# Kernel optimization log

Measured on AMD Instinct MI355X. Metric: run time of the kernel, lower is better.

## Reference

```python
import jax, jax.numpy as jnp
import numpy as np

B, C, H, W = 2, 512, 64, 64
TC = 256  # transform_channels


def _w(k, o, i):
    return jax.random.normal(k, (o, i), jnp.float32) * (1.0 / np.sqrt(i))


def setup_inputs() -> dict:
    key = jax.random.key(0)
    ks = jax.random.split(key, 8)
    ones = lambda n: jnp.ones((n,), jnp.float32)
    zeros = lambda n: jnp.zeros((n,), jnp.float32)
    return {
        "x": jax.random.normal(ks[0], (B, C, H, W), jnp.float32),
        "q_w1": _w(ks[1], TC, C), "q_g1": ones(TC), "q_b1": zeros(TC),
        "q_w2": _w(ks[2], TC, TC), "q_g2": ones(TC), "q_b2": zeros(TC),
        "k_w1": _w(ks[3], TC, 2 * C), "k_g1": ones(TC), "k_b1": zeros(TC),
        "k_w2": _w(ks[4], TC, TC), "k_g2": ones(TC), "k_b2": zeros(TC),
        "v_w": _w(ks[5], TC, 2 * C), "v_g": ones(TC), "v_b": zeros(TC),
        "o_w": _w(ks[6], C, TC), "o_g": ones(C), "o_b": zeros(C),
    }


def _proj(x, w, g, b):
    """1x1 conv (bias-free) + eval-mode BN (mean=0,var=1 -> per-ch affine) + ReLU.
    x: (B, Cin, N) -> (B, Cout, N)"""
    y = jnp.einsum('oc,bcn->bon', w, x)
    return jax.nn.relu(y * g[None, :, None] + b[None, :, None])


def reference(x, q_w1, q_g1, q_b1, q_w2, q_g2, q_b2,
              k_w1, k_g1, k_b1, k_w2, k_g2, k_b2,
              v_w, v_g, v_b, o_w, o_g, o_b):
    b, c, h, w = x.shape
    n = h * w
    xf = x.reshape(b, c, n)
    # image-level context: spatial softmax * feats, averaged over all positions
    g_vec = jnp.mean(jax.nn.softmax(xf, axis=2) * xf, axis=2)        # (b, c)
    g_map = jnp.broadcast_to(g_vec[:, :, None], (b, c, n))           # 1x1 bilinear upsample == broadcast
    kv_in = jnp.concatenate([g_map, xf], axis=1)                     # (b, 2c, n)

    q = _proj(_proj(xf, q_w1, q_g1, q_b1), q_w2, q_g2, q_b2)         # (b, tc, n)
    k = _proj(_proj(kv_in, k_w1, k_g1, k_b1), k_w2, k_g2, k_b2)      # (b, tc, n)
    v = _proj(kv_in, v_w, v_g, v_b)                                  # (b, tc, n)

    tc = q.shape[1]
    sim = jnp.einsum('bcn,bcm->bnm', q, k) * (tc ** -0.5)            # (b, n, n)
    attn = jax.nn.softmax(sim, axis=-1)
    ctx = jnp.einsum('bnm,bcm->bcn', attn, v)                        # (b, tc, n)
    out = _proj(ctx, o_w, o_g, o_b)                                  # (b, c, n)
    return out.reshape(b, -1, h, w)
```

## Files before the change

### kernel.cpp

```cpp
#include <hip/hip_runtime.h>
#include <stdint.h>

#define DEVINL __device__ __forceinline__

typedef short s16x8 __attribute__((ext_vector_type(8)));
typedef short s16x4 __attribute__((ext_vector_type(4)));
typedef float f32x4 __attribute__((ext_vector_type(4)));
typedef int   i32x4 __attribute__((ext_vector_type(4)));

DEVINL f32x4 MFMA16(s16x8 a, s16x8 b, f32x4 c) {
  return __builtin_amdgcn_mfma_f32_16x16x32_bf16(a, b, c, 0, 0, 0);
}

DEVINL short f2bf(float f) {
  uint32_t u = __float_as_uint(f);
  uint32_t r = (u + 0x7fffu + ((u >> 16) & 1u)) >> 16;
  return (short)r;
}

DEVINL int packbf(float a, float b) {
  return (int)((uint32_t)(uint16_t)f2bf(a) | ((uint32_t)(uint16_t)f2bf(b) << 16));
}

DEVINL int ab_off(int row, int kg) {
  return ((row * 128 + kg * 16) ^ ((row & 7) << 4)) >> 1;
}
DEVINL int k_off(int key, int dg) {
  return ((key * 512 + dg * 16) ^ ((key & 7) << 4)) >> 1;
}

__global__ __launch_bounds__(256) void prep_kernel(
    const float* __restrict__ x,
    const float* __restrict__ qw1, const float* __restrict__ qw2,
    const float* __restrict__ kw1, const float* __restrict__ kw2,
    const float* __restrict__ vw, const float* __restrict__ ow,
    short* __restrict__ wbuf, short* __restrict__ xt, float* __restrict__ g) {
  __shared__ float t[32][33];
  int gblk = blockIdx.x, tid = threadIdx.x;
  if (gblk < 2560) {
    int idx = gblk * 256 + tid;
    const float* src; int base, stride, coloff, sh, mask;
    if (idx < 131072)      { src = qw1; base = 0;      stride = 512;  coloff = 0;   sh = 9; mask = 511; }
    else if (idx < 196608) { src = qw2; base = 131072; stride = 256;  coloff = 0;   sh = 8; mask = 255; }
    else if (idx < 327680) { src = kw1; base = 196608; stride = 1024; coloff = 512; sh = 9; mask = 511; }
    else if (idx < 393216) { src = kw2; base = 327680; stride = 256;  coloff = 0;   sh = 8; mask = 255; }
    else if (idx < 524288) { src = vw;  base = 393216; stride = 1024; coloff = 512; sh = 9; mask = 511; }
    else                   { src = ow;  base = 524288; stride = 256;  coloff = 0;   sh = 8; mask = 255; }
    int l = idx - base;
    int r = l >> sh, c = l & mask;
    wbuf[idx] = f2bf(src[(size_t)r * stride + coloff + c]);
  } else if (gblk < 6656) {
    int g2 = gblk - 2560;
    int nt = g2 & 127, ct = (g2 >> 7) & 15, b = g2 >> 11;
    int tx = tid & 31, ty = tid >> 5;
    for (int i = 0; i < 4; ++i) {
      int c = ct * 32 + ty + i * 8;
      t[ty + i * 8][tx] = x[((size_t)(b * 512 + c)) * 4096 + nt * 32 + tx];
    }
    __syncthreads();
    for (int i = 0; i < 4; ++i) {
      int n = nt * 32 + ty + i * 8;
      xt[((size_t)(b * 4096 + n)) * 512 + ct * 32 + tx] = f2bf(t[tx][ty + i * 8]);
    }
  } else {
    int g3 = gblk - 6656;
    int c = g3 & 511, b = g3 >> 9;
    const float* row = x + ((size_t)(b * 512 + c)) * 4096;
    int w = tid >> 6, lane = tid & 63;
    float vals[16];
    float vmax = -3e38f;
    for (int i = 0; i < 4; ++i) {
      float4 v = ((const float4*)row)[tid + i * 256];
      vals[i * 4 + 0] = v.x; vals[i * 4 + 1] = v.y;
      vals[i * 4 + 2] = v.z; vals[i * 4 + 3] = v.w;
    }
    for (int i = 0; i < 16; ++i) vmax = fmaxf(vmax, vals[i]);
    for (int off = 1; off < 64; off <<= 1) vmax = fmaxf(vmax, __shfl_xor(vmax, off));
    float* sb = &t[0][0];
    if (lane == 0) sb[w] = vmax;
    __syncthreads();
    vmax = fmaxf(fmaxf(sb[0], sb[1]), fmaxf(sb[2], sb[3]));
    float se = 0.f, sex = 0.f;
    for (int i = 0; i < 16; ++i) {
      float e = __expf(vals[i] - vmax);
      se += e; sex += e * vals[i];
    }
    for (int off = 1; off < 64; off <<= 1) {
      se += __shfl_xor(se, off);
      sex += __shfl_xor(sex, off);
    }
    __syncthreads();
    if (lane == 0) { sb[4 + w] = se; sb[8 + w] = sex; }
    __syncthreads();
    if (tid == 0) {
      float tse = sb[4] + sb[5] + sb[6] + sb[7];
      float tsx = sb[8] + sb[9] + sb[10] + sb[11];
      g[b * 512 + c] = tsx / (tse * 4096.0f);
    }
  }
}

__global__ __launch_bounds__(64) void bias_kernel(const float* __restrict__ kw1,
                                                  const float* __restrict__ vw,
                                                  const float* __restrict__ g,
                                                  float* __restrict__ kbias,
                                                  float* __restrict__ vbias) {
  int o = blockIdx.x, b = blockIdx.y, which = blockIdx.z;
  const float* W = which ? vw : kw1;
  int lane = threadIdx.x;
  float s = 0.f;
  for (int j = 0; j < 8; ++j) {
    int c = lane + j * 64;
    s += W[(size_t)o * 1024 + c] * g[b * 512 + c];
  }
  for (int off = 1; off < 64; off <<= 1) s += __shfl_xor(s, off);
  if (lane == 0) (which ? vbias : kbias)[b * 256 + o] = s;
}

DEVINL void gemm_core(const short* __restrict__ Ap, const short* __restrict__ Bp,
                      int K, short* Alds, short* Blds, int tid,
                      f32x4 (&acc)[4][2]) {
  int lane = tid & 63, w = tid >> 6, lg = lane >> 4, ln = lane & 15;
  int wm = w & 1, wn = w >> 1;
  int nk = K >> 6;
  for (int kt = 0; kt < nk; ++kt) {
    int k0 = kt * 64;
#pragma unroll
    for (int j = 0; j < 4; ++j) {
      int c = tid + j * 256;
      int row = c >> 3, kg = c & 7;
      *(s16x8*)(Alds + ab_off(row, kg)) =
          *(const s16x8*)(Ap + (size_t)row * K + k0 + kg * 8);
    }
#pragma unroll
    for (int j = 0; j < 2; ++j) {
      int c = tid + j * 256;
      int row = c >> 3, kg = c & 7;
      *(s16x8*)(Blds + ab_off(row, kg)) =
          *(const s16x8*)(Bp + (size_t)row * K + k0 + kg * 8);
    }
    __syncthreads();
#pragma unroll
    for (int ks = 0; ks < 2; ++ks) {
      s16x8 af[4], bfr[2];
#pragma unroll
      for (int mi = 0; mi < 4; ++mi)
        af[mi] = *(const s16x8*)(Alds + ab_off(wm * 64 + mi * 16 + ln, ks * 4 + lg));
#pragma unroll
      for (int nj = 0; nj < 2; ++nj)
        bfr[nj] = *(const s16x8*)(Blds + ab_off(wn * 32 + nj * 16 + ln, ks * 4 + lg));
#pragma unroll
      for (int mi = 0; mi < 4; ++mi)
#pragma unroll
        for (int nj = 0; nj < 2; ++nj)
          acc[mi][nj] = MFMA16(af[mi], bfr[nj], acc[mi][nj]);
    }
    __syncthreads();
  }
}

__global__ __launch_bounds__(256) void gemm_l1(
    const short* __restrict__ xt,
    const short* __restrict__ WQ1, const short* __restrict__ WK1,
    const short* __restrict__ WV,
    const float* __restrict__ qg1, const float* __restrict__ qb1,
    const float* __restrict__ kg1, const float* __restrict__ kb1,
    const float* __restrict__ vg, const float* __restrict__ vb,
    const float* __restrict__ kbias, const float* __restrict__ vbias,
    short* __restrict__ t1, short* __restrict__ ctxS, short* __restrict__ vbuf) {
  __shared__ alignas(16) short Alds[8192];
  __shared__ alignas(16) short Blds[4096];
  int nt = blockIdx.x, mt = blockIdx.y;
  int gid = blockIdx.z >> 1, b = blockIdx.z & 1;
  const short* A; const float *gm, *bd, *cb; short* out; bool nmode;
  if (gid == 0)      { A = WQ1; gm = qg1; bd = qb1; cb = nullptr; out = t1;   nmode = true; }
  else if (gid == 1) { A = WK1; gm = kg1; bd = kb1; cb = kbias;   out = ctxS; nmode = true; }
  else               { A = WV;  gm = vg;  bd = vb;  cb = vbias;   out = vbuf; nmode = false; }
  int tid = threadIdx.x, lane = tid & 63, w = tid >> 6, lg = lane >> 4, ln = lane & 15;
  int wm = w & 1, wn = w >> 1;
  f32x4 z = {0.f, 0.f, 0.f, 0.f};
  f32x4 acc[4][2];
  for (int mi = 0; mi < 4; ++mi) for (int nj = 0; nj < 2; ++nj) acc[mi][nj] = z;
  gemm_core(A + (size_t)(mt * 128) * 512, xt + ((size_t)b * 4096 + nt * 64) * 512,
            512, Alds, Blds, tid, acc);
  for (int mi = 0; mi < 4; ++mi)
    for (int nj = 0; nj < 2; ++nj) {
      int mbase = mt * 128 + wm * 64 + mi * 16 + lg * 4;
      int n = nt * 64 + wn * 32 + nj * 16 + ln;
      if (nmode) {
        s16x4 pack;
        for (int r = 0; r < 4; ++r) {
          float a = acc[mi][nj][r];
          if (cb) a += cb[b * 256 + mbase + r];
          pack[r] = f2bf(fmaxf(a * gm[mbase + r] + bd[mbase + r], 0.f));
        }
        *(s16x4*)(out + ((size_t)b * 4096 + n) * 256 + mbase) = pack;
      } else {
        for (int r = 0; r < 4; ++r) {
          int m = mbase + r;
          float a = acc[mi][nj][r] + cb[b * 256 + m];
          out[((size_t)(b * 256 + m)) * 4096 + n] = f2bf(fmaxf(a * gm[m] + bd[m], 0.f));
        }
      }
    }
}

__global__ __launch_bounds__(256) void gemm_l2(
    const short* __restrict__ t1, const short* __restrict__ ctxS,
    const short* __restrict__ WQ2, const short* __restrict__ WK2,
    const float* __restrict__ qg2, const float* __restrict__ qb2,
    const float* __restrict__ kg2, const float* __restrict__ kb2,
    short* __restrict__ qbuf, short* __restrict__ kbuf) {
  __shared__ alignas(16) short Alds[8192];
  __shared__ alignas(16) short Blds[4096];
  int nt = blockIdx.x, mt = blockIdx.y;
  int gid = blockIdx.z >> 1, b = blockIdx.z & 1;
  const short* A = gid ? WK2 : WQ2;
  const short* B = gid ? ctxS : t1;
  const float* gm = gid ? kg2 : qg2;
  const float* bd = gid ? kb2 : qb2;
  short* out = gid ? kbuf : qbuf;
  float scale = gid ? 1.0f : 0.0625f;
  int tid = threadIdx.x, lane = tid & 63, w = tid >> 6, lg = lane >> 4, ln = lane & 15;
  int wm = w & 1, wn = w >> 1;
  f32x4 z = {0.f, 0.f, 0.f, 0.f};
  f32x4 acc[4][2];
  for (int mi = 0; mi < 4; ++mi) for (int nj = 0; nj < 2; ++nj) acc[mi][nj] = z;
  gemm_core(A + (size_t)(mt * 128) * 256, B + ((size_t)b * 4096 + nt * 64) * 256,
            256, Alds, Blds, tid, acc);
  for (int mi = 0; mi < 4; ++mi)
    for (int nj = 0; nj < 2; ++nj) {
      int mbase = mt * 128 + wm * 64 + mi * 16 + lg * 4;
      int n = nt * 64 + wn * 32 + nj * 16 + ln;
      s16x4 pack;
      for (int r = 0; r < 4; ++r) {
        float a = acc[mi][nj][r];
        pack[r] = f2bf(fmaxf(a * gm[mbase + r] + bd[mbase + r], 0.f) * scale);
      }
      *(s16x4*)(out + ((size_t)b * 4096 + n) * 256 + mbase) = pack;
    }
}

__global__ __launch_bounds__(256) void gemm_final(
    const short* __restrict__ ctx, const short* __restrict__ WO,
    const float* __restrict__ og, const float* __restrict__ ob,
    float* __restrict__ out) {
  __shared__ alignas(16) short Alds[8192];
  __shared__ alignas(16) short Blds[4096];
  int nt = blockIdx.x, mt = blockIdx.y, b = blockIdx.z;
  int tid = threadIdx.x, lane = tid & 63, w = tid >> 6, lg = lane >> 4, ln = lane & 15;
  int wm = w & 1, wn = w >> 1;
  f32x4 z = {0.f, 0.f, 0.f, 0.f};
  f32x4 acc[4][2];
  for (int mi = 0; mi < 4; ++mi) for (int nj = 0; nj < 2; ++nj) acc[mi][nj] = z;
  gemm_core(WO + (size_t)(mt * 128) * 256, ctx + ((size_t)b * 4096 + nt * 64) * 256,
            256, Alds, Blds, tid, acc);
  for (int mi = 0; mi < 4; ++mi)
    for (int nj = 0; nj < 2; ++nj) {
      int mbase = mt * 128 + wm * 64 + mi * 16 + lg * 4;
      int n = nt * 64 + wn * 32 + nj * 16 + ln;
      for (int r = 0; r < 4; ++r) {
        int m = mbase + r;
        float y = fmaxf(acc[mi][nj][r] * og[m] + ob[m], 0.f);
        out[((size_t)(b * 512 + m)) * 4096 + n] = y;
      }
    }
}

__global__ __launch_bounds__(256, 2) void attn_kernel(
    const short* __restrict__ q, const short* __restrict__ k,
    const short* __restrict__ v, float* __restrict__ accp,
    float* __restrict__ mlp, int nsplit) {
  __shared__ alignas(16) short Klds[8192];
  __shared__ alignas(16) short Vlds[8192];
  __shared__ alignas(16) short Plds[4][512];
  int qt = blockIdx.x, split = blockIdx.y, b = blockIdx.z;
  int tid = threadIdx.x, w = tid >> 6, lane = tid & 63, lg = lane >> 4, ln = lane & 15;

  const short* qrow = q + ((size_t)(b * 4096) + qt * 64 + w * 16 + ln) * 256;
  s16x8 qf[8];
#pragma unroll
  for (int kc = 0; kc < 8; ++kc) qf[kc] = *(const s16x8*)(qrow + kc * 32 + lg * 8);

  f32x4 z = {0.f, 0.f, 0.f, 0.f};
  f32x4 acc[16];
#pragma unroll
  for (int i = 0; i < 16; ++i) acc[i] = z;
  float m_run = -3e38f, l_run = 0.f;

  const size_t kvbase = (size_t)b * 4096 * 256;
  const short* kb_ = k + kvbase;
  const short* vb_ = v + kvbase;
  int kps = 4096 / nsplit;
  int ntiles = kps >> 5;
  int* pw = (int*)&Plds[w][0];

  s16x8 kst[4], vst[4];
  {
    int key0 = split * kps;
#pragma unroll
    for (int j = 0; j < 4; ++j) {
      int c = tid + j * 256;
      kst[j] = *(const s16x8*)(kb_ + (size_t)(key0 + (c >> 5)) * 256 + (c & 31) * 8);
      vst[j] = *(const s16x8*)(vb_ + (size_t)(c >> 2) * 4096 + key0 + (c & 3) * 8);
    }
  }

  for (int tile = 0; tile < ntiles; ++tile) {
#pragma unroll
    for (int j = 0; j < 4; ++j) {
      int c = tid + j * 256;
      *(s16x8*)(Klds + k_off(c >> 5, c & 31)) = kst[j];
      int d = c >> 2, kg = c & 3;
      *(s16x8*)(Vlds + (((kg * 256 + d) ^ ((kg & 1) << 2)) * 8)) = vst[j];
    }
    __syncthreads();
    if (tile + 1 < ntiles) {
      int nk0 = split * kps + (tile + 1) * 32;
#pragma unroll
      for (int j = 0; j < 4; ++j) {
        int c = tid + j * 256;
        kst[j] = *(const s16x8*)(kb_ + (size_t)(nk0 + (c >> 5)) * 256 + (c & 31) * 8);
        vst[j] = *(const s16x8*)(vb_ + (size_t)(c >> 2) * 4096 + nk0 + (c & 3) * 8);
      }
    }
    f32x4 sf0 = z, sf1 = z;
    __builtin_amdgcn_s_setprio(1);
#pragma unroll
    for (int kc = 0; kc < 8; ++kc) {
      s16x8 kb0 = *(const s16x8*)(Klds + k_off(ln, kc * 4 + lg));
      s16x8 kb1 = *(const s16x8*)(Klds + k_off(16 + ln, kc * 4 + lg));
      sf0 = MFMA16(kb0, qf[kc], sf0);
      sf1 = MFMA16(kb1, qf[kc], sf1);
    }
    __builtin_amdgcn_s_setprio(0);
    float mx = fmaxf(fmaxf(fmaxf(sf0[0], sf0[1]), fmaxf(sf0[2], sf0[3])),
                     fmaxf(fmaxf(sf1[0], sf1[1]), fmaxf(sf1[2], sf1[3])));
    mx = fmaxf(mx, __shfl_xor(mx, 16));
    mx = fmaxf(mx, __shfl_xor(mx, 32));
    if (__any(mx > m_run + 8.0f)) {
      float mnew = fmaxf(m_run, mx);
      float alpha = __expf(m_run - mnew);
      m_run = mnew;
      l_run *= alpha;
      float ar0 = __shfl(alpha, lg * 4 + 0);
      float ar1 = __shfl(alpha, lg * 4 + 1);
      float ar2 = __shfl(alpha, lg * 4 + 2);
      float ar3 = __shfl(alpha, lg * 4 + 3);
#pragma unroll
      for (int df = 0; df < 16; ++df) {
        acc[df][0] *= ar0; acc[df][1] *= ar1;
        acc[df][2] *= ar2; acc[df][3] *= ar3;
      }
    }
    float p0[4], p1[4];
    float ps = 0.f;
#pragma unroll
    for (int r = 0; r < 4; ++r) {
      p0[r] = __expf(sf0[r] - m_run);
      p1[r] = __expf(sf1[r] - m_run);
      ps += p0[r] + p1[r];
    }
    ps += __shfl_xor(ps, 16);
    ps += __shfl_xor(ps, 32);
    l_run += ps;
    int u0 = lg ^ (ln & 7);
    int u1 = (4 | lg) ^ (ln & 7);
    *(int2*)(pw + ln * 16 + u0 * 2) = make_int2(packbf(p0[0], p0[1]), packbf(p0[2], p0[3]));
    *(int2*)(pw + ln * 16 + u1 * 2) = make_int2(packbf(p1[0], p1[1]), packbf(p1[2], p1[3]));
    int2 a0 = *(int2*)(pw + ln * 16 + (((2 * lg) ^ (ln & 7)) * 2));
    int2 a1 = *(int2*)(pw + ln * 16 + (((2 * lg + 1) ^ (ln & 7)) * 2));
    i32x4 pt; pt.x = a0.x; pt.y = a0.y; pt.z = a1.x; pt.w = a1.y;
    s16x8 pa = __builtin_bit_cast(s16x8, pt);
    __builtin_amdgcn_s_setprio(1);
#pragma unroll
    for (int df = 0; df < 16; ++df) {
      int unit = (lg * 256 + df * 16 + ln) ^ ((lg & 1) << 2);
      s16x8 vb = *(const s16x8*)(Vlds + unit * 8);
      acc[df] = MFMA16(pa, vb, acc[df]);
    }
    __builtin_amdgcn_s_setprio(0);
    __syncthreads();
  }
  float* accrow = accp + (((size_t)(split * 2 + b) * 4096) + qt * 64 + w * 16) * 256;
#pragma unroll
  for (int df = 0; df < 16; ++df)
#pragma unroll
    for (int r = 0; r < 4; ++r)
      accrow[(size_t)(lg * 4 + r) * 256 + df * 16 + ln] = acc[df][r];
  if (lane < 16) {
    size_t rowi = ((size_t)(split * 2 + b) * 4096) + qt * 64 + w * 16 + ln;
    mlp[rowi * 2] = m_run;
    mlp[rowi * 2 + 1] = l_run;
  }
}

__global__ __launch_bounds__(256) void attn_merge(const float* __restrict__ accp,
                                                  const float* __restrict__ mlp,
                                                  short* __restrict__ ctx, int nsplit) {
  int tid = threadIdx.x;
  int row = blockIdx.x * 4 + (tid >> 6), b = blockIdx.y;
  int lane = tid & 63;
  float M = -3e38f;
  for (int i = 0; i < nsplit; ++i)
    M = fmaxf(M, mlp[((size_t)(i * 2 + b) * 4096 + row) * 2]);
  float denom = 0.f;
  float vx = 0.f, vy = 0.f, vz = 0.f, vw = 0.f;
  for (int i = 0; i < nsplit; ++i) {
    size_t ri = (size_t)(i * 2 + b) * 4096 + row;
    float wgt = __expf(mlp[ri * 2] - M);
    denom += wgt * mlp[ri * 2 + 1];
    float4 a = *(const float4*)(accp + ri * 256 + lane * 4);
    vx += wgt * a.x; vy += wgt * a.y; vz += wgt * a.z; vw += wgt * a.w;
  }
  float inv = 1.0f / denom;
  s16x4 pack;
  pack[0] = f2bf(vx * inv); pack[1] = f2bf(vy * inv);
  pack[2] = f2bf(vz * inv); pack[3] = f2bf(vw * inv);
  *(s16x4*)(ctx + ((size_t)b * 4096 + row) * 256 + lane * 4) = pack;
}

extern "C" void kernel_launch(void* const* d_in, const int* in_sizes, int n_in,
                              void* d_out, int out_size, void* d_ws, size_t ws_size,
                              hipStream_t stream) {
  const float* x    = (const float*)d_in[0];
  const float* qw1  = (const float*)d_in[1];
  const float* qg1  = (const float*)d_in[2];
  const float* qb1  = (const float*)d_in[3];
  const float* qw2  = (const float*)d_in[4];
  const float* qg2  = (const float*)d_in[5];
  const float* qb2  = (const float*)d_in[6];
  const float* kw1  = (const float*)d_in[7];
  const float* kg1  = (const float*)d_in[8];
  const float* kb1f = (const float*)d_in[9];
  const float* kw2  = (const float*)d_in[10];
  const float* kg2  = (const float*)d_in[11];
  const float* kb2f = (const float*)d_in[12];
  const float* vw   = (const float*)d_in[13];
  const float* vg   = (const float*)d_in[14];
  const float* vbf_ = (const float*)d_in[15];
  const float* ow   = (const float*)d_in[16];
  const float* og   = (const float*)d_in[17];
  const float* ob   = (const float*)d_in[18];
  (void)in_sizes; (void)n_in;

  char* ws = (char*)d_ws;
  size_t off = 0;
  short* wbuf = (short*)(ws + off); off += 1310720;
  short* xt   = (short*)(ws + off); off += 8388608;
  float* gvec = (float*)(ws + off); off += 4096;
  float* kbias= (float*)(ws + off); off += 4096;
  float* vbias= (float*)(ws + off); off += 4096;
  short* t1   = (short*)(ws + off); off += 4194304;
  short* qbuf = (short*)(ws + off); off += 4194304;
  short* kbuf = (short*)(ws + off); off += 4194304;
  short* vbuf = (short*)(ws + off); off += 4194304;
  short* ctx  = (short*)(ws + off); off += 4194304;
  float* mlp  = (float*)(ws + off); off += 524288;
  float* accp = (float*)(ws + off);
  size_t basesz = off;
  const size_t per = 8388608ull;
  int nsplit = 1;
  if (ws_size >= basesz + 4 * per) nsplit = 4;
  else if (ws_size >= basesz + 2 * per) nsplit = 2;
  else if (ws_size < basesz + per)
    accp = (float*)d_out;

  prep_kernel<<<7680, 256, 0, stream>>>(x, qw1, qw2, kw1, kw2, vw, ow,
                                        wbuf, xt, gvec);
  bias_kernel<<<dim3(256, 2, 2), 64, 0, stream>>>(kw1, vw, gvec, kbias, vbias);

  short* WQ1 = wbuf + 0;
  short* WQ2 = wbuf + 131072;
  short* WK1 = wbuf + 196608;
  short* WK2 = wbuf + 327680;
  short* WV  = wbuf + 393216;
  short* WO  = wbuf + 524288;

  gemm_l1<<<dim3(64, 2, 6), 256, 0, stream>>>(xt, WQ1, WK1, WV,
                                              qg1, qb1, kg1, kb1f, vg, vbf_,
                                              kbias, vbias, t1, ctx, vbuf);
  gemm_l2<<<dim3(64, 2, 4), 256, 0, stream>>>(t1, ctx, WQ2, WK2,
                                              qg2, qb2, kg2, kb2f, qbuf, kbuf);

  attn_kernel<<<dim3(64, nsplit, 2), 256, 0, stream>>>(qbuf, kbuf, vbuf, accp, mlp, nsplit);
  attn_merge<<<dim3(1024, 2), 256, 0, stream>>>(accp, mlp, ctx, nsplit);

  gemm_final<<<dim3(64, 4, 2), 256, 0, stream>>>(ctx, WO, og, ob, (float*)d_out);
}
```

Baseline: 123.4 us.

## Process two 16-row query tiles per wave in attention kernel

Each wave now handles 32 query rows (two independent online-softmax states) instead of 16, so every K and V tile staged in LDS feeds twice as many MFMAs. The grid's query dimension is halved to match. The register-staged prefetch of the next K/V tile is dropped in favour of direct global-to-LDS copies, and launch bounds are relaxed to one block per SIMD group. The costs are a doubled accumulator register footprint, lower occupancy, fewer blocks, and global load latency that is no longer hidden behind compute.

```diff
diff --git a/kernel.cpp b/kernel.cpp
--- a/kernel.cpp
+++ b/kernel.cpp
@@ -267,131 +267,138 @@
     }
 }
 
-__global__ __launch_bounds__(256, 2) void attn_kernel(
+DEVINL s16x8 softmax_pa(f32x4 sf0, f32x4 sf1, float& m_run, float& l_run,
+                        f32x4 (&acc)[16], int* pw, int lg, int ln) {
+  float mx = fmaxf(fmaxf(fmaxf(sf0[0], sf0[1]), fmaxf(sf0[2], sf0[3])),
+                   fmaxf(fmaxf(sf1[0], sf1[1]), fmaxf(sf1[2], sf1[3])));
+  mx = fmaxf(mx, __shfl_xor(mx, 16));
+  mx = fmaxf(mx, __shfl_xor(mx, 32));
+  if (__any(mx > m_run + 8.0f)) {
+    float mnew = fmaxf(m_run, mx);
+    float alpha = __expf(m_run - mnew);
+    m_run = mnew;
+    l_run *= alpha;
+    float ar0 = __shfl(alpha, lg * 4 + 0);
+    float ar1 = __shfl(alpha, lg * 4 + 1);
+    float ar2 = __shfl(alpha, lg * 4 + 2);
+    float ar3 = __shfl(alpha, lg * 4 + 3);
+#pragma unroll
+    for (int df = 0; df < 16; ++df) {
+      acc[df][0] *= ar0; acc[df][1] *= ar1;
+      acc[df][2] *= ar2; acc[df][3] *= ar3;
+    }
+  }
+  float p0[4], p1[4];
+  float ps = 0.f;
+#pragma unroll
+  for (int r = 0; r < 4; ++r) {
+    p0[r] = __expf(sf0[r] - m_run);
+    p1[r] = __expf(sf1[r] - m_run);
+    ps += p0[r] + p1[r];
+  }
+  ps += __shfl_xor(ps, 16);
+  ps += __shfl_xor(ps, 32);
+  l_run += ps;
+  int u0 = lg ^ (ln & 7);
+  int u1 = (4 | lg) ^ (ln & 7);
+  *(int2*)(pw + ln * 16 + u0 * 2) = make_int2(packbf(p0[0], p0[1]), packbf(p0[2], p0[3]));
+  *(int2*)(pw + ln * 16 + u1 * 2) = make_int2(packbf(p1[0], p1[1]), packbf(p1[2], p1[3]));
+  int2 a0 = *(int2*)(pw + ln * 16 + (((2 * lg) ^ (ln & 7)) * 2));
+  int2 a1 = *(int2*)(pw + ln * 16 + (((2 * lg + 1) ^ (ln & 7)) * 2));
+  i32x4 pt; pt.x = a0.x; pt.y = a0.y; pt.z = a1.x; pt.w = a1.y;
+  return __builtin_bit_cast(s16x8, pt);
+}
+
+__global__ __launch_bounds__(256, 1) void attn_kernel(
     const short* __restrict__ q, const short* __restrict__ k,
     const short* __restrict__ v, float* __restrict__ accp,
     float* __restrict__ mlp, int nsplit) {
   __shared__ alignas(16) short Klds[8192];
   __shared__ alignas(16) short Vlds[8192];
-  __shared__ alignas(16) short Plds[4][512];
+  __shared__ alignas(16) short Plds[4][1024];
   int qt = blockIdx.x, split = blockIdx.y, b = blockIdx.z;
   int tid = threadIdx.x, w = tid >> 6, lane = tid & 63, lg = lane >> 4, ln = lane & 15;
 
-  const short* qrow = q + ((size_t)(b * 4096) + qt * 64 + w * 16 + ln) * 256;
-  s16x8 qf[8];
-#pragma unroll
-  for (int kc = 0; kc < 8; ++kc) qf[kc] = *(const s16x8*)(qrow + kc * 32 + lg * 8);
+  const short* qrow0 = q + ((size_t)(b * 4096) + qt * 128 + w * 32 + ln) * 256;
+  const short* qrow1 = qrow0 + 16 * 256;
+  s16x8 qf0[8], qf1[8];
+#pragma unroll
+  for (int kc = 0; kc < 8; ++kc) {
+    qf0[kc] = *(const s16x8*)(qrow0 + kc * 32 + lg * 8);
+    qf1[kc] = *(const s16x8*)(qrow1 + kc * 32 + lg * 8);
+  }
 
   f32x4 z = {0.f, 0.f, 0.f, 0.f};
-  f32x4 acc[16];
-#pragma unroll
-  for (int i = 0; i < 16; ++i) acc[i] = z;
-  float m_run = -3e38f, l_run = 0.f;
+  f32x4 acc0[16], acc1[16];
+#pragma unroll
+  for (int i = 0; i < 16; ++i) { acc0[i] = z; acc1[i] = z; }
+  float m0 = -3e38f, l0 = 0.f, m1 = -3e38f, l1 = 0.f;
+
+  int* pw0 = (int*)&Plds[w][0];
+  int* pw1 = (int*)&Plds[w][512];
 
   const size_t kvbase = (size_t)b * 4096 * 256;
   const short* kb_ = k + kvbase;
   const short* vb_ = v + kvbase;
   int kps = 4096 / nsplit;
   int ntiles = kps >> 5;
-  int* pw = (int*)&Plds[w][0];
-
-  s16x8 kst[4], vst[4];
-  {
-    int key0 = split * kps;
+  for (int tile = 0; tile < ntiles; ++tile) {
+    int key0 = split * kps + tile * 32;
 #pragma unroll
     for (int j = 0; j < 4; ++j) {
       int c = tid + j * 256;
-      kst[j] = *(const s16x8*)(kb_ + (size_t)(key0 + (c >> 5)) * 256 + (c & 31) * 8);
-      vst[j] = *(const s16x8*)(vb_ + (size_t)(c >> 2) * 4096 + key0 + (c & 3) * 8);
-    }
-  }
-
-  for (int tile = 0; tile < ntiles; ++tile) {
+      *(s16x8*)(Klds + k_off(c >> 5, c & 31)) =
+          *(const s16x8*)(kb_ + (size_t)(key0 + (c >> 5)) * 256 + (c & 31) * 8);
+    }
 #pragma unroll
     for (int j = 0; j < 4; ++j) {
       int c = tid + j * 256;
-      *(s16x8*)(Klds + k_off(c >> 5, c & 31)) = kst[j];
       int d = c >> 2, kg = c & 3;
-      *(s16x8*)(Vlds + (((kg * 256 + d) ^ ((kg & 1) << 2)) * 8)) = vst[j];
-    }
-    __syncthreads();
-    if (tile + 1 < ntiles) {
-      int nk0 = split * kps + (tile + 1) * 32;
-#pragma unroll
-      for (int j = 0; j < 4; ++j) {
-        int c = tid + j * 256;
-        kst[j] = *(const s16x8*)(kb_ + (size_t)(nk0 + (c >> 5)) * 256 + (c & 31) * 8);
-        vst[j] = *(const s16x8*)(vb_ + (size_t)(c >> 2) * 4096 + nk0 + (c & 3) * 8);
-      }
-    }
-    f32x4 sf0 = z, sf1 = z;
+      int unit = (kg * 256 + d) ^ ((kg & 1) << 2);
+      *(s16x8*)(Vlds + unit * 8) =
+          *(const s16x8*)(vb_ + (size_t)d * 4096 + key0 + kg * 8);
+    }
+    __syncthreads();
+    f32x4 s00 = z, s01 = z, s10 = z, s11 = z;
     __builtin_amdgcn_s_setprio(1);
 #pragma unroll
     for (int kc = 0; kc < 8; ++kc) {
       s16x8 kb0 = *(const s16x8*)(Klds + k_off(ln, kc * 4 + lg));
       s16x8 kb1 = *(const s16x8*)(Klds + k_off(16 + ln, kc * 4 + lg));
-      sf0 = MFMA16(kb0, qf[kc], sf0);
-      sf1 = MFMA16(kb1, qf[kc], sf1);
+      s00 = MFMA16(kb0, qf0[kc], s00);
+      s01 = MFMA16(kb1, qf0[kc], s01);
+      s10 = MFMA16(kb0, qf1[kc], s10);
+      s11 = MFMA16(kb1, qf1[kc], s11);
     }
     __builtin_amdgcn_s_setprio(0);
-    float mx = fmaxf(fmaxf(fmaxf(sf0[0], sf0[1]), fmaxf(sf0[2], sf0[3])),
-                     fmaxf(fmaxf(sf1[0], sf1[1]), fmaxf(sf1[2], sf1[3])));
-    mx = fmaxf(mx, __shfl_xor(mx, 16));
-    mx = fmaxf(mx, __shfl_xor(mx, 32));
-    if (__any(mx > m_run + 8.0f)) {
-      float mnew = fmaxf(m_run, mx);
-      float alpha = __expf(m_run - mnew);
-      m_run = mnew;
-      l_run *= alpha;
-      float ar0 = __shfl(alpha, lg * 4 + 0);
-      float ar1 = __shfl(alpha, lg * 4 + 1);
-      float ar2 = __shfl(alpha, lg * 4 + 2);
-      float ar3 = __shfl(alpha, lg * 4 + 3);
-#pragma unroll
-      for (int df = 0; df < 16; ++df) {
-        acc[df][0] *= ar0; acc[df][1] *= ar1;
-        acc[df][2] *= ar2; acc[df][3] *= ar3;
-      }
-    }
-    float p0[4], p1[4];
-    float ps = 0.f;
-#pragma unroll
-    for (int r = 0; r < 4; ++r) {
-      p0[r] = __expf(sf0[r] - m_run);
-      p1[r] = __expf(sf1[r] - m_run);
-      ps += p0[r] + p1[r];
-    }
-    ps += __shfl_xor(ps, 16);
-    ps += __shfl_xor(ps, 32);
-    l_run += ps;
-    int u0 = lg ^ (ln & 7);
-    int u1 = (4 | lg) ^ (ln & 7);
-    *(int2*)(pw + ln * 16 + u0 * 2) = make_int2(packbf(p0[0], p0[1]), packbf(p0[2], p0[3]));
-    *(int2*)(pw + ln * 16 + u1 * 2) = make_int2(packbf(p1[0], p1[1]), packbf(p1[2], p1[3]));
-    int2 a0 = *(int2*)(pw + ln * 16 + (((2 * lg) ^ (ln & 7)) * 2));
-    int2 a1 = *(int2*)(pw + ln * 16 + (((2 * lg + 1) ^ (ln & 7)) * 2));
-    i32x4 pt; pt.x = a0.x; pt.y = a0.y; pt.z = a1.x; pt.w = a1.y;
-    s16x8 pa = __builtin_bit_cast(s16x8, pt);
+    s16x8 pa0 = softmax_pa(s00, s01, m0, l0, acc0, pw0, lg, ln);
+    s16x8 pa1 = softmax_pa(s10, s11, m1, l1, acc1, pw1, lg, ln);
     __builtin_amdgcn_s_setprio(1);
 #pragma unroll
     for (int df = 0; df < 16; ++df) {
       int unit = (lg * 256 + df * 16 + ln) ^ ((lg & 1) << 2);
       s16x8 vb = *(const s16x8*)(Vlds + unit * 8);
-      acc[df] = MFMA16(pa, vb, acc[df]);
+      acc0[df] = MFMA16(pa0, vb, acc0[df]);
+      acc1[df] = MFMA16(pa1, vb, acc1[df]);
     }
     __builtin_amdgcn_s_setprio(0);
     __syncthreads();
   }
-  float* accrow = accp + (((size_t)(split * 2 + b) * 4096) + qt * 64 + w * 16) * 256;
+  float* arow0 = accp + (((size_t)(split * 2 + b) * 4096) + qt * 128 + w * 32) * 256;
+  float* arow1 = arow0 + 16 * 256;
 #pragma unroll
   for (int df = 0; df < 16; ++df)
 #pragma unroll
-    for (int r = 0; r < 4; ++r)
-      accrow[(size_t)(lg * 4 + r) * 256 + df * 16 + ln] = acc[df][r];
+    for (int r = 0; r < 4; ++r) {
+      arow0[(size_t)(lg * 4 + r) * 256 + df * 16 + ln] = acc0[df][r];
+      arow1[(size_t)(lg * 4 + r) * 256 + df * 16 + ln] = acc1[df][r];
+    }
   if (lane < 16) {
-    size_t rowi = ((size_t)(split * 2 + b) * 4096) + qt * 64 + w * 16 + ln;
-    mlp[rowi * 2] = m_run;
-    mlp[rowi * 2 + 1] = l_run;
+    size_t rowi = ((size_t)(split * 2 + b) * 4096) + qt * 128 + w * 32 + ln;
+    mlp[rowi * 2] = m0;
+    mlp[rowi * 2 + 1] = l0;
+    mlp[(rowi + 16) * 2] = m1;
+    mlp[(rowi + 16) * 2 + 1] = l1;
   }
 }
 
@@ -483,7 +490,7 @@
   gemm_l2<<<dim3(64, 2, 4), 256, 0, stream>>>(t1, ctx, WQ2, WK2,
                                               qg2, qb2, kg2, kb2f, qbuf, kbuf);
 
-  attn_kernel<<<dim3(64, nsplit, 2), 256, 0, stream>>>(qbuf, kbuf, vbuf, accp, mlp, nsplit);
+  attn_kernel<<<dim3(32, nsplit, 2), 256, 0, stream>>>(qbuf, kbuf, vbuf, accp, mlp, nsplit);
   attn_merge<<<dim3(1024, 2), 256, 0, stream>>>(accp, mlp, ctx, nsplit);
 
   gemm_final<<<dim3(64, 4, 2), 256, 0, stream>>>(ctx, WO, og, ob, (float*)d_out);
```

After: 169.9 us. 1.38x slower.

## Use direct global-to-LDS async loads and double-buffer K/V tiles in attention

Applied to the files above, without the earlier changes.

Replaces the register-staged global loads plus LDS stores with `global_load_lds` async copies in both the GEMM core and the attention kernel. The XOR swizzle moves from the LDS store address to the global source address, so the LDS layout stays compatible with the existing readers. The attention kernel gets double-buffered K/V LDS tiles, which drops one barrier per tile and cuts VGPR pressure from the staging registers. In exchange it doubles K/V shared memory, which may limit occupancy, and it relies on the barrier waiting for the async LDS writes.

```diff
diff --git a/kernel.cpp b/kernel.cpp
--- a/kernel.cpp
+++ b/kernel.cpp
@@ -20,6 +20,12 @@
 
 DEVINL int packbf(float a, float b) {
   return (int)((uint32_t)(uint16_t)f2bf(a) | ((uint32_t)(uint16_t)f2bf(b) << 16));
+}
+
+DEVINL void async16(const void* g, void* l) {
+  __builtin_amdgcn_global_load_lds(
+      (const __attribute__((address_space(1))) void*)g,
+      (__attribute__((address_space(3))) void*)l, 16, 0, 0);
 }
 
 DEVINL int ab_off(int row, int kg) {
@@ -128,16 +134,16 @@
 #pragma unroll
     for (int j = 0; j < 4; ++j) {
       int c = tid + j * 256;
-      int row = c >> 3, kg = c & 7;
-      *(s16x8*)(Alds + ab_off(row, kg)) =
-          *(const s16x8*)(Ap + (size_t)row * K + k0 + kg * 8);
+      int row = c >> 3, e = c & 7;
+      async16(Ap + (size_t)row * K + k0 + ((e ^ (row & 7)) * 8),
+              Alds + (size_t)(c & ~63) * 8);
     }
 #pragma unroll
     for (int j = 0; j < 2; ++j) {
       int c = tid + j * 256;
-      int row = c >> 3, kg = c & 7;
-      *(s16x8*)(Blds + ab_off(row, kg)) =
-          *(const s16x8*)(Bp + (size_t)row * K + k0 + kg * 8);
+      int row = c >> 3, e = c & 7;
+      async16(Bp + (size_t)row * K + k0 + ((e ^ (row & 7)) * 8),
+              Blds + (size_t)(c & ~63) * 8);
     }
     __syncthreads();
 #pragma unroll
@@ -271,8 +277,8 @@
     const short* __restrict__ q, const short* __restrict__ k,
     const short* __restrict__ v, float* __restrict__ accp,
     float* __restrict__ mlp, int nsplit) {
-  __shared__ alignas(16) short Klds[8192];
-  __shared__ alignas(16) short Vlds[8192];
+  __shared__ alignas(16) short Klds[2][8192];
+  __shared__ alignas(16) short Vlds[2][8192];
   __shared__ alignas(16) short Plds[4][512];
   int qt = blockIdx.x, split = blockIdx.y, b = blockIdx.z;
   int tid = threadIdx.x, w = tid >> 6, lane = tid & 63, lg = lane >> 4, ln = lane & 15;
@@ -295,41 +301,45 @@
   int ntiles = kps >> 5;
   int* pw = (int*)&Plds[w][0];
 
-  s16x8 kst[4], vst[4];
   {
     int key0 = split * kps;
 #pragma unroll
     for (int j = 0; j < 4; ++j) {
       int c = tid + j * 256;
-      kst[j] = *(const s16x8*)(kb_ + (size_t)(key0 + (c >> 5)) * 256 + (c & 31) * 8);
-      vst[j] = *(const s16x8*)(vb_ + (size_t)(c >> 2) * 4096 + key0 + (c & 3) * 8);
-    }
-  }
-
+      int key = c >> 5, e = c & 31;
+      async16(kb_ + (size_t)(key0 + key) * 256 + ((e ^ (key & 7)) * 8),
+              &Klds[0][0] + (size_t)(c & ~63) * 8);
+      int kg = c >> 8, dd = c & 255;
+      async16(vb_ + (size_t)(dd ^ ((kg & 1) << 2)) * 4096 + key0 + kg * 8,
+              &Vlds[0][0] + (size_t)(c & ~63) * 8);
+    }
+  }
+  int cur = 0;
   for (int tile = 0; tile < ntiles; ++tile) {
-#pragma unroll
-    for (int j = 0; j < 4; ++j) {
-      int c = tid + j * 256;
-      *(s16x8*)(Klds + k_off(c >> 5, c & 31)) = kst[j];
-      int d = c >> 2, kg = c & 3;
-      *(s16x8*)(Vlds + (((kg * 256 + d) ^ ((kg & 1) << 2)) * 8)) = vst[j];
-    }
     __syncthreads();
     if (tile + 1 < ntiles) {
       int nk0 = split * kps + (tile + 1) * 32;
+      short* Kn = &Klds[cur ^ 1][0];
+      short* Vn = &Vlds[cur ^ 1][0];
 #pragma unroll
       for (int j = 0; j < 4; ++j) {
         int c = tid + j * 256;
-        kst[j] = *(const s16x8*)(kb_ + (size_t)(nk0 + (c >> 5)) * 256 + (c & 31) * 8);
-        vst[j] = *(const s16x8*)(vb_ + (size_t)(c >> 2) * 4096 + nk0 + (c & 3) * 8);
+        int key = c >> 5, e = c & 31;
+        async16(kb_ + (size_t)(nk0 + key) * 256 + ((e ^ (key & 7)) * 8),
+                Kn + (size_t)(c & ~63) * 8);
+        int kg = c >> 8, dd = c & 255;
+        async16(vb_ + (size_t)(dd ^ ((kg & 1) << 2)) * 4096 + nk0 + kg * 8,
+                Vn + (size_t)(c & ~63) * 8);
       }
     }
+    const short* Kc = &Klds[cur][0];
+    const short* Vc = &Vlds[cur][0];
     f32x4 sf0 = z, sf1 = z;
     __builtin_amdgcn_s_setprio(1);
 #pragma unroll
     for (int kc = 0; kc < 8; ++kc) {
-      s16x8 kb0 = *(const s16x8*)(Klds + k_off(ln, kc * 4 + lg));
-      s16x8 kb1 = *(const s16x8*)(Klds + k_off(16 + ln, kc * 4 + lg));
+      s16x8 kb0 = *(const s16x8*)(Kc + k_off(ln, kc * 4 + lg));
+      s16x8 kb1 = *(const s16x8*)(Kc + k_off(16 + ln, kc * 4 + lg));
       sf0 = MFMA16(kb0, qf[kc], sf0);
       sf1 = MFMA16(kb1, qf[kc], sf1);
     }
@@ -376,11 +386,11 @@
 #pragma unroll
     for (int df = 0; df < 16; ++df) {
       int unit = (lg * 256 + df * 16 + ln) ^ ((lg & 1) << 2);
-      s16x8 vb = *(const s16x8*)(Vlds + unit * 8);
+      s16x8 vb = *(const s16x8*)(Vc + unit * 8);
       acc[df] = MFMA16(pa, vb, acc[df]);
     }
     __builtin_amdgcn_s_setprio(0);
-    __syncthreads();
+    cur ^= 1;
   }
   float* accrow = accp + (((size_t)(split * 2 + b) * 4096) + qt * 64 + w * 16) * 256;
 #pragma unroll
```

Result: slower. 136.6 us (+10.7%).
